# Performance work log

Measured on AMD Instinct MI355X. Metric: run time of the kernel, lower is better.

The kernel has to match this reference:

```python
import jax, jax.numpy as jnp
import numpy as np


def setup_inputs() -> dict:
    key = jax.random.key(0)
    k1, k2, k3 = jax.random.split(key, 3)
    B, D, T, DEPTH = 16384, 512, 64, 6
    x = jax.random.normal(k1, (B, D), dtype=jnp.float32)
    # per-tree learned params, stacked over the tree axis (num_trees)
    feature_selectors = jax.random.normal(k2, (T, DEPTH, D), dtype=jnp.float32)
    thresholds = jnp.zeros((T, DEPTH), dtype=jnp.float32)
    leaf_weights = jax.random.normal(k3, (T, 2 ** DEPTH, 1), dtype=jnp.float32)
    return {"x": x, "feature_selectors": feature_selectors,
            "thresholds": thresholds, "leaf_weights": leaf_weights}


def reference(x, feature_selectors, thresholds, leaf_weights):
    # x: [B, D]; feature_selectors: [T, depth, D]; thresholds: [T, depth]
    # leaf_weights: [T, 2^depth, 1]
    B = x.shape[0]
    T, depth, _ = feature_selectors.shape
    # all trees' split logits in one GEMM: [B, T, depth]
    logits = jnp.einsum('bi,tdi->btd', x, feature_selectors) - thresholds
    probs = jax.nn.sigmoid(logits)
    # probs_stack[..., 0] = p, probs_stack[..., 1] = 1 - p  -> [B, T, depth, 2]
    probs_stack = jnp.stack([probs, 1.0 - probs], axis=-1)
    # build leaf probabilities via repeated outer products over the depth axis
    leaf = probs_stack[:, :, 0]  # [B, T, 2]
    for d in range(1, depth):
        # [B, T, 2^d, 1] * [B, T, 1, 2] -> [B, T, 2^(d+1)]
        leaf = (leaf[..., :, None] * probs_stack[:, :, d][:, :, None, :]).reshape(B, T, -1)
    # per-tree leaf_probs @ weights, summed over trees -> [B, 1]
    out = jnp.einsum('btl,tlo->bo', leaf, leaf_weights)
    return out
```

## Files before the change

### kernel.cpp

```cpp
#include <hip/hip_runtime.h>


#define DD     512
#define NCOL   384
#define NDEPTH 6
#define PKELT  (NCOL * DD)
#define XSTR   522
#define PRSTR  392

typedef __bf16 bf16_t;
typedef __bf16 bf16x8 __attribute__((ext_vector_type(8)));
typedef __bf16 bf16x4 __attribute__((ext_vector_type(4)));
typedef float  f32x4  __attribute__((ext_vector_type(4)));

static __device__ __forceinline__ float b2f(unsigned int u16) {
  unsigned int t = u16 << 16;
  float f;
  __builtin_memcpy(&f, &t, 4);
  return f;
}

__global__ __launch_bounds__(256) void node_pack(const float* __restrict__ fsel,
                                                 bf16_t* __restrict__ pk)
{
  int tid  = blockIdx.x * 256 + threadIdx.x;
  int lane = tid & 63;
  int ksg  = (tid >> 6) & 15;
  int cf   = tid >> 10;
  int col  = cf * 16 + (lane & 15);
  int k    = ksg * 32 + (lane >> 4) * 8;
  float4 f0 = *reinterpret_cast<const float4*>(fsel + (size_t)col * DD + k);
  float4 f1 = *reinterpret_cast<const float4*>(fsel + (size_t)col * DD + k + 4);
  bf16x8 v;
  v[0] = (bf16_t)f0.x; v[1] = (bf16_t)f0.y; v[2] = (bf16_t)f0.z; v[3] = (bf16_t)f0.w;
  v[4] = (bf16_t)f1.x; v[5] = (bf16_t)f1.y; v[6] = (bf16_t)f1.z; v[7] = (bf16_t)f1.w;
  #pragma unroll
  for (int c = 0; c < 8; ++c)
    *reinterpret_cast<bf16x8*>(pk + (size_t)c * PKELT + (size_t)tid * 8) = v;
}

__global__ __launch_bounds__(512) void node_fused(
    const float*  __restrict__ x,
    const bf16_t* __restrict__ pk,
    const float*  __restrict__ thr,
    const float*  __restrict__ lw,
    float*        __restrict__ out)
{
  __shared__ bf16_t xs[64 * XSTR];
  __shared__ bf16_t pr[64 * PRSTR];

  const int tid  = threadIdx.x;
  const int lane = tid & 63;
  const int wv   = tid >> 6;
  const int rowblk = blockIdx.x * 64;
  const int c   = lane & 15;
  const int kg  = lane >> 4;
  const bf16_t* pkc = pk + (size_t)(blockIdx.x & 7) * PKELT;

  float4 s0[8], s1[8];
  #pragma unroll
  for (int i = 0; i < 8; ++i) {
    int idx = i * 512 + tid, e = idx << 2, r = e >> 8, k = e & 255;
    s0[i] = *reinterpret_cast<const float4*>(x + (size_t)(rowblk + r) * DD + k);
  }
  #pragma unroll
  for (int i = 0; i < 8; ++i) {
    int idx = i * 512 + tid, e = idx << 2, r = e >> 8, k = e & 255;
    s1[i] = *reinterpret_cast<const float4*>(x + (size_t)(rowblk + r) * DD + 256 + k);
  }
  #pragma unroll
  for (int i = 0; i < 8; ++i) {
    int idx = i * 512 + tid, e = idx << 2, r = e >> 8, k = e & 255;
    bf16x4 v;
    v[0] = (bf16_t)s0[i].x; v[1] = (bf16_t)s0[i].y;
    v[2] = (bf16_t)s0[i].z; v[3] = (bf16_t)s0[i].w;
    *reinterpret_cast<bf16x4*>(&xs[r * XSTR + k]) = v;
  }
  asm volatile("s_waitcnt lgkmcnt(0)" ::: "memory");
  __builtin_amdgcn_s_barrier();

  float th[3];
  #pragma unroll
  for (int f = 0; f < 3; ++f) th[f] = thr[wv * 48 + f * 16 + c];

  f32x4 acc[4][3];
  #pragma unroll
  for (int t = 0; t < 4; ++t)
    #pragma unroll
    for (int f = 0; f < 3; ++f) acc[t][f] = (f32x4){0.f, 0.f, 0.f, 0.f};

  #pragma unroll
  for (int ch = 0; ch < 8; ++ch) {
    if (ch == 4) {
      #pragma unroll
      for (int i = 0; i < 8; ++i) {
        int idx = i * 512 + tid, e = idx << 2, r = e >> 8, k = e & 255;
        bf16x4 v;
        v[0] = (bf16_t)s1[i].x; v[1] = (bf16_t)s1[i].y;
        v[2] = (bf16_t)s1[i].z; v[3] = (bf16_t)s1[i].w;
        *reinterpret_cast<bf16x4*>(&xs[r * XSTR + 256 + k]) = v;
      }
      asm volatile("s_waitcnt lgkmcnt(0)" ::: "memory");
      __builtin_amdgcn_s_barrier();
    }

    bf16x8 bh[3][2];
    #pragma unroll
    for (int f = 0; f < 3; ++f)
      #pragma unroll
      for (int ks = 0; ks < 2; ++ks)
        bh[f][ks] = *reinterpret_cast<const bf16x8*>(
            pkc + ((size_t)(((wv * 3 + f) * 16 + ch * 2 + ks) * 64) + lane) * 8);

    #pragma unroll
    for (int t = 0; t < 4; ++t) {
      #pragma unroll
      for (int ks = 0; ks < 2; ++ks) {
        bf16x8 a = *reinterpret_cast<const bf16x8*>(
            &xs[(t * 16 + c) * XSTR + ch * 64 + ks * 32 + kg * 8]);
        acc[t][0] = __builtin_amdgcn_mfma_f32_16x16x32_bf16(a, bh[0][ks], acc[t][0], 0, 0, 0);
        acc[t][1] = __builtin_amdgcn_mfma_f32_16x16x32_bf16(a, bh[1][ks], acc[t][1], 0, 0, 0);
        acc[t][2] = __builtin_amdgcn_mfma_f32_16x16x32_bf16(a, bh[2][ks], acc[t][2], 0, 0, 0);
      }
    }
  }

  #pragma unroll
  for (int t = 0; t < 4; ++t) {
    #pragma unroll
    for (int f = 0; f < 3; ++f) {
      const int col = wv * 48 + f * 16 + c;
      #pragma unroll
      for (int r = 0; r < 4; ++r) {
        const int row = t * 16 + kg * 4 + r;
        float z = acc[t][f][r] - th[f];
        float p = 1.0f / (1.0f + __expf(-z));
        pr[row * PRSTR + col] = (bf16_t)p;
      }
    }
  }
  asm volatile("s_waitcnt lgkmcnt(0)" ::: "memory");
  __builtin_amdgcn_s_barrier();

  float p0v[8], hv0[8], hv1[8];
  #pragma unroll
  for (int half = 0; half < 2; ++half) {
    float wch[32];
    #pragma unroll
    for (int j = 0; j < 8; ++j) {
      float4 f4 = *reinterpret_cast<const float4*>(lw + (size_t)lane * 64 + half * 32 + j * 4);
      wch[4*j] = f4.x; wch[4*j+1] = f4.y; wch[4*j+2] = f4.z; wch[4*j+3] = f4.w;
    }
    #pragma unroll
    for (int rr = 0; rr < 8; ++rr) {
      const int row = wv * 8 + rr;
      const unsigned int* prow =
          reinterpret_cast<const unsigned int*>(&pr[row * PRSTR]) + lane * 3;
      unsigned int d0 = prow[0], d1 = prow[1], d2 = prow[2];
      float p1 = b2f(d0 >> 16);
      float p2 = b2f(d1 & 0xffffu), p3 = b2f(d1 >> 16);
      float p4 = b2f(d2 & 0xffffu), p5 = b2f(d2 >> 16);
      if (half == 0) p0v[rr] = b2f(d0 & 0xffffu);

      float v[16];
      #pragma unroll
      for (int j = 0; j < 16; ++j) v[j] = fmaf(p5, wch[2*j] - wch[2*j+1], wch[2*j+1]);
      #pragma unroll
      for (int j = 0; j < 8;  ++j) v[j] = fmaf(p4, v[2*j] - v[2*j+1], v[2*j+1]);
      #pragma unroll
      for (int j = 0; j < 4;  ++j) v[j] = fmaf(p3, v[2*j] - v[2*j+1], v[2*j+1]);
      #pragma unroll
      for (int j = 0; j < 2;  ++j) v[j] = fmaf(p2, v[2*j] - v[2*j+1], v[2*j+1]);
      float s = fmaf(p1, v[0] - v[1], v[1]);
      if (half == 0) hv0[rr] = s; else hv1[rr] = s;
    }
  }

  float tvv[8];
  #pragma unroll
  for (int rr = 0; rr < 8; ++rr)
    tvv[rr] = fmaf(p0v[rr], hv0[rr] - hv1[rr], hv1[rr]);

  #pragma unroll
  for (int off = 32; off; off >>= 1) {
    #pragma unroll
    for (int rr = 0; rr < 8; ++rr) tvv[rr] += __shfl_xor(tvv[rr], off, 64);
  }
  if (lane == 0) {
    #pragma unroll
    for (int rr = 0; rr < 8; ++rr) out[rowblk + wv * 8 + rr] = tvv[rr];
  }
}

extern "C" void kernel_launch(void* const* d_in, const int* in_sizes, int n_in,
                              void* d_out, int out_size, void* d_ws, size_t ws_size,
                              hipStream_t stream) {
  const float* x    = (const float*)d_in[0];
  const float* fsel = (const float*)d_in[1];
  const float* thr  = (const float*)d_in[2];
  const float* lw   = (const float*)d_in[3];
  float* out = (float*)d_out;

  bf16_t* pk = (bf16_t*)d_ws;

  const int B = in_sizes[0] / DD;

  node_pack<<<dim3(96), dim3(256), 0, stream>>>(fsel, pk);
  node_fused<<<dim3(B / 64), dim3(512), 0, stream>>>(x, pk, thr, lw, out);
}
```

Before: 27.59 us.

## Software-pipeline x staging and B-fragment loads across K chunks

Replaces the up-front bulk load of x (two halves held in 64 registers) with a double-buffered per-chunk staging scheme. Global loads for chunk n+2 are issued while chunk n is computed, and the bf16 conversion into LDS happens one chunk ahead. B fragments are prefetched for the next chunk after the MFMAs, and launch bounds request 2 blocks per SM to cut register pressure. The cost is a barrier per chunk instead of two in total, plus possible register spills under the tighter bound.

```diff
diff --git a/kernel.cpp b/kernel.cpp
--- a/kernel.cpp
+++ b/kernel.cpp
@@ -3,7 +3,6 @@
 
 #define DD     512
 #define NCOL   384
-#define NDEPTH 6
 #define PKELT  (NCOL * DD)
 #define XSTR   522
 #define PRSTR  392
@@ -39,7 +38,7 @@
     *reinterpret_cast<bf16x8*>(pk + (size_t)c * PKELT + (size_t)tid * 8) = v;
 }
 
-__global__ __launch_bounds__(512) void node_fused(
+__global__ __launch_bounds__(512, 2) void node_fused(
     const float*  __restrict__ x,
     const bf16_t* __restrict__ pk,
     const float*  __restrict__ thr,
@@ -55,33 +54,59 @@
   const int rowblk = blockIdx.x * 64;
   const int c   = lane & 15;
   const int kg  = lane >> 4;
-  const bf16_t* pkc = pk + (size_t)(blockIdx.x & 7) * PKELT;
-
-  float4 s0[8], s1[8];
-  #pragma unroll
-  for (int i = 0; i < 8; ++i) {
-    int idx = i * 512 + tid, e = idx << 2, r = e >> 8, k = e & 255;
-    s0[i] = *reinterpret_cast<const float4*>(x + (size_t)(rowblk + r) * DD + k);
-  }
-  #pragma unroll
-  for (int i = 0; i < 8; ++i) {
-    int idx = i * 512 + tid, e = idx << 2, r = e >> 8, k = e & 255;
-    s1[i] = *reinterpret_cast<const float4*>(x + (size_t)(rowblk + r) * DD + 256 + k);
-  }
-  #pragma unroll
-  for (int i = 0; i < 8; ++i) {
-    int idx = i * 512 + tid, e = idx << 2, r = e >> 8, k = e & 255;
-    bf16x4 v;
-    v[0] = (bf16_t)s0[i].x; v[1] = (bf16_t)s0[i].y;
-    v[2] = (bf16_t)s0[i].z; v[3] = (bf16_t)s0[i].w;
-    *reinterpret_cast<bf16x4*>(&xs[r * XSTR + k]) = v;
-  }
+
+  const float* xr0 = x + (size_t)(rowblk + (tid >> 4)) * DD + ((tid & 15) << 2);
+  const float* xr1 = xr0 + (size_t)32 * DD;
+  bf16_t* xw0 = &xs[(tid >> 4) * XSTR + ((tid & 15) << 2)];
+  bf16_t* xw1 = &xs[((tid >> 4) + 32) * XSTR + ((tid & 15) << 2)];
+
+  float th[3];
+  #pragma unroll
+  for (int f = 0; f < 3; ++f) th[f] = thr[wv * 48 + f * 16 + c];
+
+  float4 stg[2][2];
+
+  #define ISSUE(n, buf)                                                         \
+    do {                                                                        \
+      int off_ = (n) * 64;                                                      \
+      asm volatile("" : "+v"(off_));                                            \
+      stg[buf][0] = *reinterpret_cast<const float4*>(xr0 + off_);               \
+      stg[buf][1] = *reinterpret_cast<const float4*>(xr1 + off_);               \
+    } while (0)
+
+  #define WRITE(n, buf)                                                         \
+    do {                                                                        \
+      bf16x4 v0_, v1_;                                                          \
+      v0_[0]=(bf16_t)stg[buf][0].x; v0_[1]=(bf16_t)stg[buf][0].y;               \
+      v0_[2]=(bf16_t)stg[buf][0].z; v0_[3]=(bf16_t)stg[buf][0].w;               \
+      v1_[0]=(bf16_t)stg[buf][1].x; v1_[1]=(bf16_t)stg[buf][1].y;               \
+      v1_[2]=(bf16_t)stg[buf][1].z; v1_[3]=(bf16_t)stg[buf][1].w;               \
+      *reinterpret_cast<bf16x4*>(xw0 + (n) * 64) = v0_;                         \
+      *reinterpret_cast<bf16x4*>(xw1 + (n) * 64) = v1_;                         \
+    } while (0)
+
+  bf16x8 bh[3][2];
+  #define LOAD_BH(n)                                                            \
+    do {                                                                        \
+      const bf16_t* q_ = pk + (size_t)(blockIdx.x & 7) * PKELT +                \
+                         (size_t)lane * 8 + (size_t)(n) * 1024 +                \
+                         (size_t)wv * 3 * 8192;                                 \
+      asm volatile("" : "+v"(q_));                                              \
+      _Pragma("unroll")                                                         \
+      for (int f_ = 0; f_ < 3; ++f_)                                            \
+        _Pragma("unroll")                                                       \
+        for (int ks_ = 0; ks_ < 2; ++ks_)                                       \
+          bh[f_][ks_] = *reinterpret_cast<const bf16x8*>(                       \
+              q_ + f_ * 8192 + ks_ * 512);                                      \
+    } while (0)
+
+  ISSUE(0, 0);
+  ISSUE(1, 1);
+  WRITE(0, 0);
+  ISSUE(2, 0);
   asm volatile("s_waitcnt lgkmcnt(0)" ::: "memory");
   __builtin_amdgcn_s_barrier();
-
-  float th[3];
-  #pragma unroll
-  for (int f = 0; f < 3; ++f) th[f] = thr[wv * 48 + f * 16 + c];
+  LOAD_BH(0);
 
   f32x4 acc[4][3];
   #pragma unroll
@@ -91,27 +116,6 @@
 
   #pragma unroll
   for (int ch = 0; ch < 8; ++ch) {
-    if (ch == 4) {
-      #pragma unroll
-      for (int i = 0; i < 8; ++i) {
-        int idx = i * 512 + tid, e = idx << 2, r = e >> 8, k = e & 255;
-        bf16x4 v;
-        v[0] = (bf16_t)s1[i].x; v[1] = (bf16_t)s1[i].y;
-        v[2] = (bf16_t)s1[i].z; v[3] = (bf16_t)s1[i].w;
-        *reinterpret_cast<bf16x4*>(&xs[r * XSTR + 256 + k]) = v;
-      }
-      asm volatile("s_waitcnt lgkmcnt(0)" ::: "memory");
-      __builtin_amdgcn_s_barrier();
-    }
-
-    bf16x8 bh[3][2];
-    #pragma unroll
-    for (int f = 0; f < 3; ++f)
-      #pragma unroll
-      for (int ks = 0; ks < 2; ++ks)
-        bh[f][ks] = *reinterpret_cast<const bf16x8*>(
-            pkc + ((size_t)(((wv * 3 + f) * 16 + ch * 2 + ks) * 64) + lane) * 8);
-
     #pragma unroll
     for (int t = 0; t < 4; ++t) {
       #pragma unroll
@@ -123,7 +127,17 @@
         acc[t][2] = __builtin_amdgcn_mfma_f32_16x16x32_bf16(a, bh[2][ks], acc[t][2], 0, 0, 0);
       }
     }
-  }
+    if (ch < 7) {
+      LOAD_BH(ch + 1);
+      WRITE(ch + 1, (ch + 1) & 1);
+      if (ch < 5) ISSUE(ch + 3, (ch + 1) & 1);
+      asm volatile("s_waitcnt lgkmcnt(0)" ::: "memory");
+      __builtin_amdgcn_s_barrier();
+    }
+  }
+  #undef ISSUE
+  #undef WRITE
+  #undef LOAD_BH
 
   #pragma unroll
   for (int t = 0; t < 4; ++t) {
```

After: 27.27 us. About the same (-1.2%).
